# Kernel tuning notes

Hardware: AMD Instinct MI355X
Metric: run time of the kernel (lower is better)

The kernel has to match this reference:

```python
import jax, jax.numpy as jnp
import numpy as np

N_NODES = 100000
N_EDGES = 1600000
IN_DIM = 128
HID = 32
HEADS = 4
OUT_DIM = 32


def gat_conv(x, W, al, ar, b, src, dst, apply_elu):
    """DGL-style GATConv. x:[N,F_in], W:[F_in,H*D], al/ar/b:[H,D]."""
    N = x.shape[0]
    H, D = al.shape
    f = (x @ W).reshape(N, H, D)                      # projected features [N,H,D]
    el = jnp.sum(f * al, axis=-1)                     # [N,H]
    er = jnp.sum(f * ar, axis=-1)                     # [N,H]
    e = jax.nn.leaky_relu(el[src] + er[dst], 0.2)     # per-edge scores [E,H]
    # segment softmax over incoming edges of each dst node
    m = jax.ops.segment_max(e, dst, num_segments=N)   # [N,H]
    m = jnp.where(jnp.isfinite(m), m, 0.0)            # zero-in-degree safety
    w = jnp.exp(e - m[dst])                           # [E,H]
    s = jax.ops.segment_sum(w, dst, num_segments=N)   # [N,H]
    alpha = w / jnp.maximum(s[dst], 1e-9)             # [E,H]
    out = jax.ops.segment_sum(alpha[:, :, None] * f[src], dst, num_segments=N)  # [N,H,D]
    out = out + b
    if apply_elu:
        out = jax.nn.elu(out)
    return out


def setup_inputs() -> dict:
    key = jax.random.key(0)
    ks = jax.random.split(key, 16)
    sc = 0.05
    HD = HEADS * HID
    return {
        "x": jax.random.normal(ks[0], (N_NODES, IN_DIM), jnp.float32),
        "src": jax.random.randint(ks[1], (N_EDGES,), 0, N_NODES, jnp.int32),
        "dst": jax.random.randint(ks[2], (N_EDGES,), 0, N_NODES, jnp.int32),
        "W1": jax.random.normal(ks[3], (IN_DIM, HD), jnp.float32) * sc,
        "al1": jax.random.normal(ks[4], (HEADS, HID), jnp.float32) * sc,
        "ar1": jax.random.normal(ks[5], (HEADS, HID), jnp.float32) * sc,
        "b1": jnp.zeros((HEADS, HID), jnp.float32),
        "W2": jax.random.normal(ks[6], (HD, HD), jnp.float32) * sc,
        "al2": jax.random.normal(ks[7], (HEADS, HID), jnp.float32) * sc,
        "ar2": jax.random.normal(ks[8], (HEADS, HID), jnp.float32) * sc,
        "b2": jnp.zeros((HEADS, HID), jnp.float32),
        "W3": jax.random.normal(ks[9], (HD, OUT_DIM), jnp.float32) * sc,
        "al3": jax.random.normal(ks[10], (1, OUT_DIM), jnp.float32) * sc,
        "ar3": jax.random.normal(ks[11], (1, OUT_DIM), jnp.float32) * sc,
        "b3": jnp.zeros((1, OUT_DIM), jnp.float32),
    }


def reference(x, src, dst, W1, al1, ar1, b1, W2, al2, ar2, b2, W3, al3, ar3, b3):
    h = gat_conv(x, W1, al1, ar1, b1, src, dst, apply_elu=True)
    h = h.reshape(h.shape[0], -1)                     # concat heads [N, H*D]
    h = gat_conv(h, W2, al2, ar2, b2, src, dst, apply_elu=True)
    h = h.reshape(h.shape[0], -1)
    h = gat_conv(h, W3, al3, ar3, b3, src, dst, apply_elu=False)
    return h.squeeze(1)                               # [N, OUT_DIM]
```

## Files before the change

### kernel.cpp

```cpp
#include <hip/hip_runtime.h>
#include <hip/hip_bf16.h>

#define IN_DIM 128
#define HDIM 128


__global__ __launch_bounds__(256) void hist_kernel(const int* __restrict__ dst,
                                                   int* __restrict__ deg, int E) {
  int e = blockIdx.x * 256 + threadIdx.x;
  if (e < E) atomicAdd(&deg[dst[e]], 1);
}

__global__ __launch_bounds__(512) void scan1_kernel(const int* __restrict__ deg,
                                                    int* __restrict__ partial,
                                                    int* __restrict__ bsum, int n) {
  __shared__ int sm[512];
  int g = blockIdx.x * 512 + threadIdx.x;
  int v = (g < n) ? deg[g] : 0;
  sm[threadIdx.x] = v;
  __syncthreads();
  for (int off = 1; off < 512; off <<= 1) {
    int t = (threadIdx.x >= off) ? sm[threadIdx.x - off] : 0;
    __syncthreads();
    sm[threadIdx.x] += t;
    __syncthreads();
  }
  if (g < n) partial[g] = sm[threadIdx.x];
  if (threadIdx.x == 511) bsum[blockIdx.x] = sm[511];
}

__global__ __launch_bounds__(512) void scan2_kernel(int* __restrict__ bsum, int nblk) {
  __shared__ int sm[512];
  int v = (threadIdx.x < nblk) ? bsum[threadIdx.x] : 0;
  sm[threadIdx.x] = v;
  __syncthreads();
  for (int off = 1; off < 512; off <<= 1) {
    int t = (threadIdx.x >= off) ? sm[threadIdx.x - off] : 0;
    __syncthreads();
    sm[threadIdx.x] += t;
    __syncthreads();
  }
  if (threadIdx.x < nblk) bsum[threadIdx.x] = sm[threadIdx.x];
}

__global__ __launch_bounds__(512) void scanfix_kernel(const int* __restrict__ partial,
                                                      const int* __restrict__ bsum,
                                                      const int* __restrict__ deg,
                                                      int* __restrict__ row_ptr,
                                                      int* __restrict__ cursor, int n) {
  int g = blockIdx.x * 512 + threadIdx.x;
  if (g >= n) return;
  int off = (blockIdx.x > 0) ? bsum[blockIdx.x - 1] : 0;
  int incl = partial[g] + off;
  row_ptr[g + 1] = incl;
  cursor[g] = incl - deg[g];
  if (g == 0) row_ptr[0] = 0;
}

__global__ __launch_bounds__(256) void scatter_kernel(const int* __restrict__ src,
                                                      const int* __restrict__ dst,
                                                      int* __restrict__ cursor,
                                                      int* __restrict__ col, int E) {
  int e = blockIdx.x * 256 + threadIdx.x;
  if (e >= E) return;
  int d = dst[e];
  int p = atomicAdd(&cursor[d], 1);
  col[p] = src[e];
}


__global__ __launch_bounds__(256) void gemm128_kernel(const float* __restrict__ X,
                                                      const float* __restrict__ W,
                                                      const float* __restrict__ al,
                                                      const float* __restrict__ ar,
                                                      float* __restrict__ Fout,
                                                      float* __restrict__ el,
                                                      float* __restrict__ er, int n) {
  __shared__ float As[16][132];
  __shared__ float Bs[16][128];
  const int tid = threadIdx.x;
  const int tm = tid >> 4, tn = tid & 15;
  const int bm = blockIdx.x * 128;
  float acc[8][8];
#pragma unroll
  for (int i = 0; i < 8; ++i)
#pragma unroll
    for (int j = 0; j < 8; ++j) acc[i][j] = 0.f;

  for (int kc = 0; kc < 128; kc += 16) {
#pragma unroll
    for (int jj = 0; jj < 2; ++jj) {
      int rl = (tid >> 2) + jj * 64;
      int c4 = (tid & 3) * 4;
      int row = bm + rl;
      float4 v = make_float4(0.f, 0.f, 0.f, 0.f);
      if (row < n) v = *(const float4*)&X[(size_t)row * IN_DIM + kc + c4];
      As[c4 + 0][rl] = v.x; As[c4 + 1][rl] = v.y;
      As[c4 + 2][rl] = v.z; As[c4 + 3][rl] = v.w;
    }
#pragma unroll
    for (int jj = 0; jj < 2; ++jj) {
      int idx = tid + jj * 256;
      int kr = idx >> 5;
      int c4 = (idx & 31) * 4;
      *(float4*)&Bs[kr][c4] = *(const float4*)&W[(size_t)(kc + kr) * HDIM + c4];
    }
    __syncthreads();
#pragma unroll
    for (int k = 0; k < 16; ++k) {
      float4 a0 = *(const float4*)&As[k][tm * 8];
      float4 a1 = *(const float4*)&As[k][tm * 8 + 4];
      float4 b0 = *(const float4*)&Bs[k][tn * 8];
      float4 b1 = *(const float4*)&Bs[k][tn * 8 + 4];
      float av[8] = {a0.x, a0.y, a0.z, a0.w, a1.x, a1.y, a1.z, a1.w};
      float bv[8] = {b0.x, b0.y, b0.z, b0.w, b1.x, b1.y, b1.z, b1.w};
#pragma unroll
      for (int i = 0; i < 8; ++i)
#pragma unroll
        for (int j = 0; j < 8; ++j) acc[i][j] = fmaf(av[i], bv[j], acc[i][j]);
    }
    __syncthreads();
  }
#pragma unroll
  for (int i = 0; i < 8; ++i) {
    int row = bm + tm * 8 + i;
    if (row < n) {
      float4 v0 = make_float4(acc[i][0], acc[i][1], acc[i][2], acc[i][3]);
      float4 v1 = make_float4(acc[i][4], acc[i][5], acc[i][6], acc[i][7]);
      *(float4*)&Fout[(size_t)row * HDIM + tn * 8] = v0;
      *(float4*)&Fout[(size_t)row * HDIM + tn * 8 + 4] = v1;
    }
  }
  const int hh = tn >> 2;
  const int c0 = (tn & 3) * 8;
  float alq[8], arq[8];
#pragma unroll
  for (int j = 0; j < 8; ++j) {
    alq[j] = al[hh * 32 + c0 + j];
    arq[j] = ar[hh * 32 + c0 + j];
  }
#pragma unroll
  for (int i = 0; i < 8; ++i) {
    float pl = 0.f, pr = 0.f;
#pragma unroll
    for (int j = 0; j < 8; ++j) {
      pl = fmaf(acc[i][j], alq[j], pl);
      pr = fmaf(acc[i][j], arq[j], pr);
    }
    pl += __shfl_xor(pl, 1); pl += __shfl_xor(pl, 2);
    pr += __shfl_xor(pr, 1); pr += __shfl_xor(pr, 2);
    int row = bm + tm * 8 + i;
    if ((tn & 3) == 0 && row < n) {
      el[row * 4 + hh] = pl;
      er[row * 4 + hh] = pr;
    }
  }
}

__global__ __launch_bounds__(256) void gemm_n32_kernel(const float* __restrict__ X,
                                                       const float* __restrict__ W,
                                                       const float* __restrict__ al,
                                                       const float* __restrict__ ar,
                                                       float* __restrict__ Fout,
                                                       float* __restrict__ el,
                                                       float* __restrict__ er, int n) {
  __shared__ float Xs[32][132];
  __shared__ float Ws[128][32];
  const int tid = threadIdx.x;
  const int row0 = blockIdx.x * 32;
#pragma unroll
  for (int jj = 0; jj < 4; ++jj) {
    int idx = tid + jj * 256;
    int r = idx >> 3;
    int c4 = (idx & 7) * 4;
    *(float4*)&Ws[r][c4] = *(const float4*)&W[(size_t)r * 32 + c4];
  }
#pragma unroll
  for (int jj = 0; jj < 4; ++jj) {
    int idx = tid + jj * 256;
    int r = idx >> 5;
    int c4 = (idx & 31) * 4;
    int row = row0 + r;
    float4 v = make_float4(0.f, 0.f, 0.f, 0.f);
    if (row < n) v = *(const float4*)&X[(size_t)row * HDIM + c4];
    *(float4*)&Xs[r][c4] = v;
  }
  __syncthreads();
  const int r = tid >> 3, cg = (tid & 7) * 4;
  float4 acc = make_float4(0.f, 0.f, 0.f, 0.f);
#pragma unroll 8
  for (int k = 0; k < 128; ++k) {
    float a = Xs[r][k];
    float4 b = *(const float4*)&Ws[k][cg];
    acc.x = fmaf(a, b.x, acc.x); acc.y = fmaf(a, b.y, acc.y);
    acc.z = fmaf(a, b.z, acc.z); acc.w = fmaf(a, b.w, acc.w);
  }
  int row = row0 + r;
  if (row < n) *(float4*)&Fout[(size_t)row * 32 + cg] = acc;
  float pl = acc.x * al[cg] + acc.y * al[cg + 1] + acc.z * al[cg + 2] + acc.w * al[cg + 3];
  float pr = acc.x * ar[cg] + acc.y * ar[cg + 1] + acc.z * ar[cg + 2] + acc.w * ar[cg + 3];
  pl += __shfl_xor(pl, 1); pl += __shfl_xor(pl, 2); pl += __shfl_xor(pl, 4);
  pr += __shfl_xor(pr, 1); pr += __shfl_xor(pr, 2); pr += __shfl_xor(pr, 4);
  if ((tid & 7) == 0 && row < n) { el[row] = pl; er[row] = pr; }
}


template <int H, int D, bool ELU>
__global__ __launch_bounds__(256) void aggregate_kernel(const float* __restrict__ f,
                                                        const float* __restrict__ el,
                                                        const float* __restrict__ er,
                                                        const float* __restrict__ bias,
                                                        const int* __restrict__ row_ptr,
                                                        const int* __restrict__ col,
                                                        float* __restrict__ out, int n) {
  constexpr int F = H * D;
  constexpr int LPN = F / 4;
  constexpr int NPB = 256 / LPN;
  int node = blockIdx.x * NPB + threadIdx.x / LPN;
  int ll = threadIdx.x % LPN;
  if (node >= n) return;
  const int h = (4 * ll) / D;
  const float er_n = er[node * H + h];
  int beg = row_ptr[node], end = row_ptr[node + 1];

  float ssum = 0.f;
  float4 acc = make_float4(0.f, 0.f, 0.f, 0.f);

  constexpr int U = 8;
  if (beg < end) {
    int s[U];
#pragma unroll
    for (int j = 0; j < U; ++j) {
      int idx = beg + j; idx = (idx < end) ? idx : (end - 1);
      s[j] = col[idx];
    }
    for (int i = beg; i < end; i += U) {
      float4 fv[U];
#pragma unroll
      for (int j = 0; j < U; ++j) fv[j] = *(const float4*)&f[(size_t)s[j] * F + 4 * ll];
      float elv[U];
#pragma unroll
      for (int j = 0; j < U; ++j) elv[j] = el[s[j] * H + h];
      int sn[U];
      int inext = i + U;
#pragma unroll
      for (int j = 0; j < U; ++j) {
        int idx = inext + j; idx = (idx < end) ? idx : (end - 1);
        sn[j] = col[idx];
      }
#pragma unroll
      for (int j = 0; j < U; ++j) {
        float e = elv[j] + er_n;
        e = (e > 0.f) ? e : 0.2f * e;
        float w = ((i + j) < end) ? __expf(e) : 0.f;
        ssum += w;
        acc.x = fmaf(w, fv[j].x, acc.x);
        acc.y = fmaf(w, fv[j].y, acc.y);
        acc.z = fmaf(w, fv[j].z, acc.z);
        acc.w = fmaf(w, fv[j].w, acc.w);
      }
#pragma unroll
      for (int j = 0; j < U; ++j) s[j] = sn[j];
    }
  }

  float inv = 1.f / fmaxf(ssum, 1e-9f);
  float4 bb = *(const float4*)&bias[4 * ll];
  float4 o;
  o.x = acc.x * inv + bb.x;
  o.y = acc.y * inv + bb.y;
  o.z = acc.z * inv + bb.z;
  o.w = acc.w * inv + bb.w;
  if (ELU) {
    o.x = (o.x > 0.f) ? o.x : (__expf(o.x) - 1.f);
    o.y = (o.y > 0.f) ? o.y : (__expf(o.y) - 1.f);
    o.z = (o.z > 0.f) ? o.z : (__expf(o.z) - 1.f);
    o.w = (o.w > 0.f) ? o.w : (__expf(o.w) - 1.f);
  }
  *(float4*)&out[(size_t)node * F + 4 * ll] = o;
}


extern "C" void kernel_launch(void* const* d_in, const int* in_sizes, int n_in,
                              void* d_out, int out_size, void* d_ws, size_t ws_size,
                              hipStream_t stream) {
  const float* x   = (const float*)d_in[0];
  const int*   src = (const int*)d_in[1];
  const int*   dst = (const int*)d_in[2];
  const float* W1  = (const float*)d_in[3];
  const float* al1 = (const float*)d_in[4];
  const float* ar1 = (const float*)d_in[5];
  const float* b1  = (const float*)d_in[6];
  const float* W2  = (const float*)d_in[7];
  const float* al2 = (const float*)d_in[8];
  const float* ar2 = (const float*)d_in[9];
  const float* b2  = (const float*)d_in[10];
  const float* W3  = (const float*)d_in[11];
  const float* al3 = (const float*)d_in[12];
  const float* ar3 = (const float*)d_in[13];
  const float* b3  = (const float*)d_in[14];
  float* out = (float*)d_out;

  const int N = in_sizes[0] / IN_DIM;
  const int E = in_sizes[1];

  char* w = (char*)d_ws;
  size_t off = 0;
  auto alloc = [&](size_t bytes) -> void* {
    void* p = w + off;
    off += (bytes + 255) & ~(size_t)255;
    return p;
  };
  int*   deg     = (int*)alloc((size_t)N * 4);
  int*   row_ptr = (int*)alloc((size_t)(N + 1) * 4);
  int*   cursor  = (int*)alloc((size_t)N * 4);
  int*   bsum    = (int*)alloc(4096);
  int*   col     = (int*)alloc((size_t)E * 4);
  float* el      = (float*)alloc((size_t)N * 4 * 4);
  float* er      = (float*)alloc((size_t)N * 4 * 4);
  float* bufA    = (float*)alloc((size_t)N * 128 * 4);
  float* bufB    = (float*)alloc((size_t)N * 128 * 4);

  hipMemsetAsync(deg, 0, (size_t)N * 4, stream);
  hist_kernel<<<(E + 255) / 256, 256, 0, stream>>>(dst, deg, E);
  int nblk = (N + 511) / 512;
  scan1_kernel<<<nblk, 512, 0, stream>>>(deg, cursor, bsum, N);
  scan2_kernel<<<1, 512, 0, stream>>>(bsum, nblk);
  scanfix_kernel<<<nblk, 512, 0, stream>>>(cursor, bsum, deg, row_ptr, cursor, N);
  scatter_kernel<<<(E + 255) / 256, 256, 0, stream>>>(src, dst, cursor, col, E);

  const int gb = (N + 127) / 128;
  gemm128_kernel<<<gb, 256, 0, stream>>>(x, W1, al1, ar1, bufA, el, er, N);
  aggregate_kernel<4, 32, true><<<(N + 7) / 8, 256, 0, stream>>>(bufA, el, er, b1, row_ptr, col, bufB, N);
  gemm128_kernel<<<gb, 256, 0, stream>>>(bufB, W2, al2, ar2, bufA, el, er, N);
  aggregate_kernel<4, 32, true><<<(N + 7) / 8, 256, 0, stream>>>(bufA, el, er, b2, row_ptr, col, bufB, N);
  gemm_n32_kernel<<<(N + 31) / 32, 256, 0, stream>>>(bufB, W3, al3, ar3, bufA, el, er, N);
  aggregate_kernel<1, 32, false><<<(N + 31) / 32, 256, 0, stream>>>(bufA, el, er, b3, row_ptr, col, out, N);
}
```

Baseline: 731.7 us.

## Use split-bf16 MFMA GEMMs with hi/lo activation buffers

Replaces the FP32 SIMT 128x128 GEMM with an MFMA bf16 kernel that emulates near-FP32 precision by splitting inputs and weights into hi/lo bf16 parts and issuing three MFMAs per tile. Weights are pre-swizzled into fragment layout, and aggregation kernels now write activations directly as hi/lo bf16 pairs to feed the next GEMM. The aggregation loop is also restructured to drop the software-prefetch tail masking in favour of a full-unroll main loop plus scalar remainder. Adds a split pass over x and extra kernel launches, and loads A fragments directly from global without LDS staging.

```diff
diff --git a/kernel.cpp b/kernel.cpp
--- a/kernel.cpp
+++ b/kernel.cpp
@@ -3,6 +3,23 @@
 
 #define IN_DIM 128
 #define HDIM 128
+
+typedef __attribute__((ext_vector_type(8))) short bf16x8;
+typedef __attribute__((ext_vector_type(4))) float f32x4;
+typedef __attribute__((ext_vector_type(4))) unsigned short ushort4v;
+
+__device__ __forceinline__ float bf2f(unsigned short h) {
+  union { unsigned u; float f; } a; a.u = ((unsigned)h) << 16; return a.f;
+}
+__device__ __forceinline__ unsigned short f2bf(float x) {
+  union { float f; unsigned u; } a; a.f = x;
+  unsigned r = a.u + 0x7FFFu + ((a.u >> 16) & 1u);
+  return (unsigned short)(r >> 16);
+}
+__device__ __forceinline__ void bfsplit(float x, unsigned short& h, unsigned short& l) {
+  h = f2bf(x);
+  l = f2bf(x - bf2f(h));
+}
 
 
 __global__ __launch_bounds__(256) void hist_kernel(const int* __restrict__ dst,
@@ -69,95 +86,129 @@
 }
 
 
-__global__ __launch_bounds__(256) void gemm128_kernel(const float* __restrict__ X,
-                                                      const float* __restrict__ W,
-                                                      const float* __restrict__ al,
-                                                      const float* __restrict__ ar,
-                                                      float* __restrict__ Fout,
-                                                      float* __restrict__ el,
-                                                      float* __restrict__ er, int n) {
-  __shared__ float As[16][132];
-  __shared__ float Bs[16][128];
-  const int tid = threadIdx.x;
-  const int tm = tid >> 4, tn = tid & 15;
+__global__ __launch_bounds__(256) void split_kernel(const float* __restrict__ x,
+                                                    unsigned short* __restrict__ xhi,
+                                                    unsigned short* __restrict__ xlo,
+                                                    int total4) {
+  int idx = blockIdx.x * 256 + threadIdx.x;
+  if (idx >= total4) return;
+  float4 v = *(const float4*)&x[(size_t)idx * 4];
+  ushort4v h, l;
+  unsigned short a, b;
+  bfsplit(v.x, a, b); h.x = a; l.x = b;
+  bfsplit(v.y, a, b); h.y = a; l.y = b;
+  bfsplit(v.z, a, b); h.z = a; l.z = b;
+  bfsplit(v.w, a, b); h.w = a; l.w = b;
+  *(ushort4v*)&xhi[(size_t)idx * 4] = h;
+  *(ushort4v*)&xlo[(size_t)idx * 4] = l;
+}
+
+
+__global__ __launch_bounds__(64) void wfrag_kernel(const float* __restrict__ W, int HD, int NB,
+                                                   unsigned short* __restrict__ whi,
+                                                   unsigned short* __restrict__ wlo) {
+  int fb = blockIdx.x;
+  int l = threadIdx.x;
+  int kb = fb / NB, nb = fb % NB;
+  unsigned short hi[8], lo[8];
+#pragma unroll
+  for (int j = 0; j < 8; ++j) {
+    int k = kb * 32 + (l >> 4) * 8 + j;
+    int c = nb * 16 + (l & 15);
+    bfsplit(W[(size_t)k * HD + c], hi[j], lo[j]);
+  }
+  size_t off = ((size_t)fb * 64 + l) * 8;
+#pragma unroll
+  for (int j = 0; j < 8; ++j) { whi[off + j] = hi[j]; wlo[off + j] = lo[j]; }
+}
+
+
+__global__ __launch_bounds__(256) void gemm128_mfma_kernel(
+    const unsigned short* __restrict__ xhi, const unsigned short* __restrict__ xlo,
+    const unsigned short* __restrict__ whi, const unsigned short* __restrict__ wlo,
+    const float* __restrict__ al, const float* __restrict__ ar,
+    float* __restrict__ F, float* __restrict__ el, float* __restrict__ er, int n) {
+  const int lane = threadIdx.x & 63;
+  const int w = threadIdx.x >> 6;
   const int bm = blockIdx.x * 128;
-  float acc[8][8];
-#pragma unroll
-  for (int i = 0; i < 8; ++i)
-#pragma unroll
-    for (int j = 0; j < 8; ++j) acc[i][j] = 0.f;
-
-  for (int kc = 0; kc < 128; kc += 16) {
-#pragma unroll
-    for (int jj = 0; jj < 2; ++jj) {
-      int rl = (tid >> 2) + jj * 64;
-      int c4 = (tid & 3) * 4;
-      int row = bm + rl;
-      float4 v = make_float4(0.f, 0.f, 0.f, 0.f);
-      if (row < n) v = *(const float4*)&X[(size_t)row * IN_DIM + kc + c4];
-      As[c4 + 0][rl] = v.x; As[c4 + 1][rl] = v.y;
-      As[c4 + 2][rl] = v.z; As[c4 + 3][rl] = v.w;
-    }
-#pragma unroll
-    for (int jj = 0; jj < 2; ++jj) {
-      int idx = tid + jj * 256;
-      int kr = idx >> 5;
-      int c4 = (idx & 31) * 4;
-      *(float4*)&Bs[kr][c4] = *(const float4*)&W[(size_t)(kc + kr) * HDIM + c4];
-    }
-    __syncthreads();
-#pragma unroll
-    for (int k = 0; k < 16; ++k) {
-      float4 a0 = *(const float4*)&As[k][tm * 8];
-      float4 a1 = *(const float4*)&As[k][tm * 8 + 4];
-      float4 b0 = *(const float4*)&Bs[k][tn * 8];
-      float4 b1 = *(const float4*)&Bs[k][tn * 8 + 4];
-      float av[8] = {a0.x, a0.y, a0.z, a0.w, a1.x, a1.y, a1.z, a1.w};
-      float bv[8] = {b0.x, b0.y, b0.z, b0.w, b1.x, b1.y, b1.z, b1.w};
-#pragma unroll
-      for (int i = 0; i < 8; ++i)
-#pragma unroll
-        for (int j = 0; j < 8; ++j) acc[i][j] = fmaf(av[i], bv[j], acc[i][j]);
-    }
-    __syncthreads();
-  }
-#pragma unroll
-  for (int i = 0; i < 8; ++i) {
-    int row = bm + tm * 8 + i;
-    if (row < n) {
-      float4 v0 = make_float4(acc[i][0], acc[i][1], acc[i][2], acc[i][3]);
-      float4 v1 = make_float4(acc[i][4], acc[i][5], acc[i][6], acc[i][7]);
-      *(float4*)&Fout[(size_t)row * HDIM + tn * 8] = v0;
-      *(float4*)&Fout[(size_t)row * HDIM + tn * 8 + 4] = v1;
-    }
-  }
-  const int hh = tn >> 2;
-  const int c0 = (tn & 3) * 8;
-  float alq[8], arq[8];
-#pragma unroll
-  for (int j = 0; j < 8; ++j) {
-    alq[j] = al[hh * 32 + c0 + j];
-    arq[j] = ar[hh * 32 + c0 + j];
-  }
-#pragma unroll
-  for (int i = 0; i < 8; ++i) {
-    float pl = 0.f, pr = 0.f;
-#pragma unroll
-    for (int j = 0; j < 8; ++j) {
-      pl = fmaf(acc[i][j], alq[j], pl);
-      pr = fmaf(acc[i][j], arq[j], pr);
-    }
-    pl += __shfl_xor(pl, 1); pl += __shfl_xor(pl, 2);
-    pr += __shfl_xor(pr, 1); pr += __shfl_xor(pr, 2);
-    int row = bm + tm * 8 + i;
-    if ((tn & 3) == 0 && row < n) {
-      el[row * 4 + hh] = pl;
-      er[row * 4 + hh] = pr;
-    }
-  }
-}
-
-__global__ __launch_bounds__(256) void gemm_n32_kernel(const float* __restrict__ X,
+  const int lr = lane & 15;
+  const int lk = lane >> 4;
+
+  f32x4 acc[2][8];
+#pragma unroll
+  for (int mf = 0; mf < 2; ++mf)
+#pragma unroll
+    for (int nb = 0; nb < 8; ++nb) acc[mf][nb] = (f32x4){0.f, 0.f, 0.f, 0.f};
+
+  int arow[2];
+#pragma unroll
+  for (int mf = 0; mf < 2; ++mf) {
+    int r = bm + w * 32 + mf * 16 + lr;
+    arow[mf] = (r < n) ? r : (n - 1);
+  }
+
+  for (int kb = 0; kb < 4; ++kb) {
+    bf16x8 ah[2], alo2[2];
+#pragma unroll
+    for (int mf = 0; mf < 2; ++mf) {
+      size_t ab = (size_t)arow[mf] * 128 + kb * 32 + lk * 8;
+      ah[mf] = *(const bf16x8*)(xhi + ab);
+      alo2[mf] = *(const bf16x8*)(xlo + ab);
+    }
+#pragma unroll
+    for (int nb = 0; nb < 8; ++nb) {
+      size_t wb = ((size_t)(kb * 8 + nb) * 64 + lane) * 8;
+      bf16x8 bh = *(const bf16x8*)(whi + wb);
+      bf16x8 bl = *(const bf16x8*)(wlo + wb);
+#pragma unroll
+      for (int mf = 0; mf < 2; ++mf) {
+        acc[mf][nb] = __builtin_amdgcn_mfma_f32_16x16x32_bf16(ah[mf], bh, acc[mf][nb], 0, 0, 0);
+        acc[mf][nb] = __builtin_amdgcn_mfma_f32_16x16x32_bf16(ah[mf], bl, acc[mf][nb], 0, 0, 0);
+        acc[mf][nb] = __builtin_amdgcn_mfma_f32_16x16x32_bf16(alo2[mf], bh, acc[mf][nb], 0, 0, 0);
+      }
+    }
+  }
+
+  float alv[4][2], arv[4][2];
+#pragma unroll
+  for (int hh = 0; hh < 4; ++hh)
+#pragma unroll
+    for (int p = 0; p < 2; ++p) {
+      alv[hh][p] = al[hh * 32 + p * 16 + lr];
+      arv[hh][p] = ar[hh * 32 + p * 16 + lr];
+    }
+
+#pragma unroll
+  for (int mf = 0; mf < 2; ++mf) {
+#pragma unroll
+    for (int r = 0; r < 4; ++r) {
+      int grow = bm + w * 32 + mf * 16 + lk * 4 + r;
+      bool ok = grow < n;
+      if (ok) {
+#pragma unroll
+        for (int nb = 0; nb < 8; ++nb)
+          F[(size_t)grow * HDIM + nb * 16 + lr] = acc[mf][nb][r];
+      }
+#pragma unroll
+      for (int hh = 0; hh < 4; ++hh) {
+        float pl = acc[mf][2 * hh][r] * alv[hh][0] + acc[mf][2 * hh + 1][r] * alv[hh][1];
+        float pr = acc[mf][2 * hh][r] * arv[hh][0] + acc[mf][2 * hh + 1][r] * arv[hh][1];
+        pl += __shfl_xor(pl, 1); pl += __shfl_xor(pl, 2);
+        pl += __shfl_xor(pl, 4); pl += __shfl_xor(pl, 8);
+        pr += __shfl_xor(pr, 1); pr += __shfl_xor(pr, 2);
+        pr += __shfl_xor(pr, 4); pr += __shfl_xor(pr, 8);
+        if (ok && lr == 0) {
+          el[grow * 4 + hh] = pl;
+          er[grow * 4 + hh] = pr;
+        }
+      }
+    }
+  }
+}
+
+
+__global__ __launch_bounds__(256) void gemm_n32_kernel(const unsigned short* __restrict__ Xhi,
+                                                       const unsigned short* __restrict__ Xlo,
                                                        const float* __restrict__ W,
                                                        const float* __restrict__ al,
                                                        const float* __restrict__ ar,
@@ -181,9 +232,16 @@
     int r = idx >> 5;
     int c4 = (idx & 31) * 4;
     int row = row0 + r;
-    float4 v = make_float4(0.f, 0.f, 0.f, 0.f);
-    if (row < n) v = *(const float4*)&X[(size_t)row * HDIM + c4];
-    *(float4*)&Xs[r][c4] = v;
+    if (row < n) {
+      ushort4v h = *(const ushort4v*)&Xhi[(size_t)row * HDIM + c4];
+      ushort4v l = *(const ushort4v*)&Xlo[(size_t)row * HDIM + c4];
+      Xs[r][c4 + 0] = bf2f(h.x) + bf2f(l.x);
+      Xs[r][c4 + 1] = bf2f(h.y) + bf2f(l.y);
+      Xs[r][c4 + 2] = bf2f(h.z) + bf2f(l.z);
+      Xs[r][c4 + 3] = bf2f(h.w) + bf2f(l.w);
+    } else {
+      Xs[r][c4 + 0] = 0.f; Xs[r][c4 + 1] = 0.f; Xs[r][c4 + 2] = 0.f; Xs[r][c4 + 3] = 0.f;
+    }
   }
   __syncthreads();
   const int r = tid >> 3, cg = (tid & 7) * 4;
@@ -205,14 +263,17 @@
 }
 
 
-template <int H, int D, bool ELU>
+template <int H, int D, bool ELU, bool OSPLIT>
 __global__ __launch_bounds__(256) void aggregate_kernel(const float* __restrict__ f,
                                                         const float* __restrict__ el,
                                                         const float* __restrict__ er,
                                                         const float* __restrict__ bias,
                                                         const int* __restrict__ row_ptr,
                                                         const int* __restrict__ col,
-                                                        float* __restrict__ out, int n) {
+                                                        float* __restrict__ out,
+                                                        unsigned short* __restrict__ ohi,
+                                                        unsigned short* __restrict__ olo,
+                                                        int n) {
   constexpr int F = H * D;
   constexpr int LPN = F / 4;
   constexpr int NPB = 256 / LPN;
@@ -227,41 +288,40 @@
   float4 acc = make_float4(0.f, 0.f, 0.f, 0.f);
 
   constexpr int U = 8;
-  if (beg < end) {
+  int i = beg;
+  for (; i + U <= end; i += U) {
     int s[U];
 #pragma unroll
+    for (int j = 0; j < U; ++j) s[j] = col[i + j];
+    float4 fv[U];
+#pragma unroll
+    for (int j = 0; j < U; ++j) fv[j] = *(const float4*)&f[(size_t)s[j] * F + 4 * ll];
+    float elv[U];
+#pragma unroll
+    for (int j = 0; j < U; ++j) elv[j] = el[s[j] * H + h];
+#pragma unroll
     for (int j = 0; j < U; ++j) {
-      int idx = beg + j; idx = (idx < end) ? idx : (end - 1);
-      s[j] = col[idx];
-    }
-    for (int i = beg; i < end; i += U) {
-      float4 fv[U];
-#pragma unroll
-      for (int j = 0; j < U; ++j) fv[j] = *(const float4*)&f[(size_t)s[j] * F + 4 * ll];
-      float elv[U];
-#pragma unroll
-      for (int j = 0; j < U; ++j) elv[j] = el[s[j] * H + h];
-      int sn[U];
-      int inext = i + U;
-#pragma unroll
-      for (int j = 0; j < U; ++j) {
-        int idx = inext + j; idx = (idx < end) ? idx : (end - 1);
-        sn[j] = col[idx];
-      }
-#pragma unroll
-      for (int j = 0; j < U; ++j) {
-        float e = elv[j] + er_n;
-        e = (e > 0.f) ? e : 0.2f * e;
-        float w = ((i + j) < end) ? __expf(e) : 0.f;
-        ssum += w;
-        acc.x = fmaf(w, fv[j].x, acc.x);
-        acc.y = fmaf(w, fv[j].y, acc.y);
-        acc.z = fmaf(w, fv[j].z, acc.z);
-        acc.w = fmaf(w, fv[j].w, acc.w);
-      }
-#pragma unroll
-      for (int j = 0; j < U; ++j) s[j] = sn[j];
-    }
+      float e = elv[j] + er_n;
+      e = (e > 0.f) ? e : 0.2f * e;
+      float wgt = __expf(e);
+      ssum += wgt;
+      acc.x = fmaf(wgt, fv[j].x, acc.x);
+      acc.y = fmaf(wgt, fv[j].y, acc.y);
+      acc.z = fmaf(wgt, fv[j].z, acc.z);
+      acc.w = fmaf(wgt, fv[j].w, acc.w);
+    }
+  }
+  for (; i < end; ++i) {
+    int s = col[i];
+    float e = el[s * H + h] + er_n;
+    e = (e > 0.f) ? e : 0.2f * e;
+    float wgt = __expf(e);
+    float4 fv = *(const float4*)&f[(size_t)s * F + 4 * ll];
+    ssum += wgt;
+    acc.x = fmaf(wgt, fv.x, acc.x);
+    acc.y = fmaf(wgt, fv.y, acc.y);
+    acc.z = fmaf(wgt, fv.z, acc.z);
+    acc.w = fmaf(wgt, fv.w, acc.w);
   }
 
   float inv = 1.f / fmaxf(ssum, 1e-9f);
@@ -277,7 +337,18 @@
     o.z = (o.z > 0.f) ? o.z : (__expf(o.z) - 1.f);
     o.w = (o.w > 0.f) ? o.w : (__expf(o.w) - 1.f);
   }
-  *(float4*)&out[(size_t)node * F + 4 * ll] = o;
+  if (OSPLIT) {
+    ushort4v hi, lo;
+    unsigned short a, b;
+    bfsplit(o.x, a, b); hi.x = a; lo.x = b;
+    bfsplit(o.y, a, b); hi.y = a; lo.y = b;
+    bfsplit(o.z, a, b); hi.z = a; lo.z = b;
+    bfsplit(o.w, a, b); hi.w = a; lo.w = b;
+    *(ushort4v*)&ohi[(size_t)node * F + 4 * ll] = hi;
+    *(ushort4v*)&olo[(size_t)node * F + 4 * ll] = lo;
+  } else {
+    *(float4*)&out[(size_t)node * F + 4 * ll] = o;
+  }
 }
 
 
@@ -319,7 +390,16 @@
   float* el      = (float*)alloc((size_t)N * 4 * 4);
   float* er      = (float*)alloc((size_t)N * 4 * 4);
   float* bufA    = (float*)alloc((size_t)N * 128 * 4);
-  float* bufB    = (float*)alloc((size_t)N * 128 * 4);
+  unsigned short* bhi = (unsigned short*)alloc((size_t)N * 128 * 2);
+  unsigned short* blo = (unsigned short*)alloc((size_t)N * 128 * 2);
+  unsigned short* w1hi = (unsigned short*)alloc(4 * 8 * 64 * 8 * 2);
+  unsigned short* w1lo = (unsigned short*)alloc(4 * 8 * 64 * 8 * 2);
+  unsigned short* w2hi = (unsigned short*)alloc(4 * 8 * 64 * 8 * 2);
+  unsigned short* w2lo = (unsigned short*)alloc(4 * 8 * 64 * 8 * 2);
+
+  wfrag_kernel<<<32, 64, 0, stream>>>(W1, HDIM, 8, w1hi, w1lo);
+  wfrag_kernel<<<32, 64, 0, stream>>>(W2, HDIM, 8, w2hi, w2lo);
+  split_kernel<<<(N * 128 / 4 + 255) / 256, 256, 0, stream>>>(x, bhi, blo, N * 128 / 4);
 
   hipMemsetAsync(deg, 0, (size_t)N * 4, stream);
   hist_kernel<<<(E + 255) / 256, 256, 0, stream>>>(dst, deg, E);
@@ -330,10 +410,13 @@
   scatter_kernel<<<(E + 255) / 256, 256, 0, stream>>>(src, dst, cursor, col, E);
 
   const int gb = (N + 127) / 128;
-  gemm128_kernel<<<gb, 256, 0, stream>>>(x, W1, al1, ar1, bufA, el, er, N);
-  aggregate_kernel<4, 32, true><<<(N + 7) / 8, 256, 0, stream>>>(bufA, el, er, b1, row_ptr, col, bufB, N);
-  gemm128_kernel<<<gb, 256, 0, stream>>>(bufB, W2, al2, ar2, bufA, el, er, N);
-  aggregate_kernel<4, 32, true><<<(N + 7) / 8, 256, 0, stream>>>(bufA, el, er, b2, row_ptr, col, bufB, N);
-  gemm_n32_kernel<<<(N + 31) / 32, 256, 0, stream>>>(bufB, W3, al3, ar3, bufA, el, er, N);
-  aggregate_kernel<1, 32, false><<<(N + 31) / 32, 256, 0, stream>>>(bufA, el, er, b3, row_ptr, col, out, N);
-}
+  gemm128_mfma_kernel<<<gb, 256, 0, stream>>>(bhi, blo, w1hi, w1lo, al1, ar1, bufA, el, er, N);
+  aggregate_kernel<4, 32, true, true><<<(N + 7) / 8, 256, 0, stream>>>(
+      bufA, el, er, b1, row_ptr, col, nullptr, bhi, blo, N);
+  gemm128_mfma_kernel<<<gb, 256, 0, stream>>>(bhi, blo, w2hi, w2lo, al2, ar2, bufA, el, er, N);
+  aggregate_kernel<4, 32, true, true><<<(N + 7) / 8, 256, 0, stream>>>(
+      bufA, el, er, b2, row_ptr, col, nullptr, bhi, blo, N);
+  gemm_n32_kernel<<<(N + 31) / 32, 256, 0, stream>>>(bhi, blo, W3, al3, ar3, bufA, el, er, N);
+  aggregate_kernel<1, 32, false, false><<<(N + 31) / 32, 256, 0, stream>>>(
+      bufA, el, er, b3, row_ptr, col, out, nullptr, nullptr, N);
+}
```

After: 726.9 us. No clear change (-0.7%).
